# Kernel optimization log

Measured on AMD Instinct MI355X. Metric: run time of the kernel, lower is better.

## Reference

```python
import jax, jax.numpy as jnp
import numpy as np

N_HEADS = 12


def setup_inputs() -> dict:
    key = jax.random.key(0)
    ks = jax.random.split(key, 4)
    B, T, C = 1, 4096, 768
    x = jax.random.normal(ks[0], (B, T, C), dtype=jnp.float32)
    w_qkv = jax.random.normal(ks[1], (C, 3 * C), dtype=jnp.float32) * (C ** -0.5)
    b_qkv = jnp.zeros((3 * C,), dtype=jnp.float32)
    w_proj = jax.random.normal(ks[2], (C, C), dtype=jnp.float32) * (C ** -0.5)
    b_proj = jnp.zeros((C,), dtype=jnp.float32)
    return {"x": x, "w_qkv": w_qkv, "b_qkv": b_qkv, "w_proj": w_proj, "b_proj": b_proj}


def reference(x, w_qkv, b_qkv, w_proj, b_proj):
    B, T, C = x.shape
    H = N_HEADS
    hd = C // H
    qkv = x @ w_qkv + b_qkv                      # [B,T,3C]
    q, k, v = jnp.split(qkv, 3, axis=-1)
    # [B,H,T,hd]
    q = q.reshape(B, T, H, hd).transpose(0, 2, 1, 3)
    k = k.reshape(B, T, H, hd).transpose(0, 2, 1, 3)
    v = v.reshape(B, T, H, hd).transpose(0, 2, 1, 3)
    scale = 1.0 / jnp.sqrt(jnp.float32(hd))
    attn = jnp.einsum('bhqd,bhkd->bhqk', q, k) * scale  # [B,H,T,T]
    causal = jnp.tril(jnp.ones((T, T), dtype=bool))
    attn = jnp.where(causal, attn, jnp.float32(-jnp.inf))
    attn = jax.nn.softmax(attn, axis=-1)
    out = jnp.einsum('bhqk,bhkd->bhqd', attn, v)        # [B,H,T,hd]
    out = out.transpose(0, 2, 1, 3).reshape(B, T, C)
    return out @ w_proj + b_proj
```

## Files before the change

kernel.cpp:

```cpp
#include <hip/hip_runtime.h>
#include <hip/hip_bf16.h>


#define T_SEQ 4096
#define C_DIM 768
#define C3    2304
#define NH    12
#define HD    64

typedef __attribute__((ext_vector_type(8))) short bf16x8;
typedef __attribute__((ext_vector_type(4))) short bf16x4;
typedef __attribute__((ext_vector_type(4))) float f32x4;

__device__ inline unsigned short f2bf(float f) {
  union { float f; unsigned u; } v; v.f = f;
  unsigned r = v.u + 0x7fff + ((v.u >> 16) & 1);
  return (unsigned short)(r >> 16);
}
__device__ inline unsigned pack_bf16_trunc(float a, float b) {
  union { float f; unsigned u; } x, y; x.f = a; y.f = b;
  return (x.u >> 16) | (y.u & 0xffff0000u);
}

__device__ inline void gl2lds16(const void* g, void* l) {
  __builtin_amdgcn_global_load_lds(
      (const __attribute__((address_space(1))) unsigned int*)g,
      (__attribute__((address_space(3))) unsigned int*)l, 16, 0, 0);
}

#if __has_builtin(__builtin_amdgcn_exp2f)
#define EXP2F(x) __builtin_amdgcn_exp2f(x)
#else
#define EXP2F(x) exp2f(x)
#endif

#define NB_CONV  (T_SEQ * C_DIM / 2048)
#define NB_TQKV  ((C3 / 32) * (C_DIM / 32))
#define NB_TPROJ ((C_DIM / 32) * (C_DIM / 32))

__global__ __launch_bounds__(256) void prep_fused(
    const float* __restrict__ x, const float* __restrict__ w_qkv,
    const float* __restrict__ w_proj, unsigned short* __restrict__ xb,
    unsigned short* __restrict__ wqkvT, unsigned short* __restrict__ wprojT) {
  __shared__ float t[32][33];
  const int b = blockIdx.x;
  const int tid = threadIdx.x;

  if (b < NB_CONV) {
    int i = (b * 256 + tid) * 8;
    float4 v0 = *(const float4*)(x + i);
    float4 v1 = *(const float4*)(x + i + 4);
    unsigned short o[8] = {f2bf(v0.x), f2bf(v0.y), f2bf(v0.z), f2bf(v0.w),
                           f2bf(v1.x), f2bf(v1.y), f2bf(v1.z), f2bf(v1.w)};
    *(uint4*)(xb + i) = *(uint4*)o;
    return;
  }
  const float* in;
  unsigned short* outT;
  int R, Cc, bi;
  if (b < NB_CONV + NB_TQKV) {
    in = w_qkv; outT = wqkvT; R = C_DIM; Cc = C3; bi = b - NB_CONV;
  } else {
    in = w_proj; outT = wprojT; R = C_DIM; Cc = C_DIM; bi = b - NB_CONV - NB_TQKV;
  }
  const int tx = tid & 31, ty = tid >> 5;
  const int c0 = (bi % (Cc / 32)) * 32, r0 = (bi / (Cc / 32)) * 32;
#pragma unroll
  for (int i = 0; i < 4; ++i) {
    int r = ty + i * 8;
    t[r][tx] = in[(size_t)(r0 + r) * Cc + c0 + tx];
  }
  __syncthreads();
#pragma unroll
  for (int i = 0; i < 4; ++i) {
    int c = ty + i * 8;
    outT[(size_t)(c0 + c) * R + r0 + tx] = f2bf(t[tx][c]);
  }
}

__global__ __launch_bounds__(256) void gemm_qkv(
    const unsigned short* __restrict__ A, const unsigned short* __restrict__ Bt,
    const float* __restrict__ bias, unsigned short* __restrict__ Cq,
    unsigned short* __restrict__ vTp, int M, int N, int K) {
  __shared__ unsigned short As[128 * 32];
  __shared__ unsigned short Bs[128 * 32];
  const int tid = threadIdx.x;
  const int wave = tid >> 6, lane = tid & 63;
  const int lo = lane & 15, g8 = lane >> 4;
  const int wm = wave >> 1, wn = wave & 1;
  const int bm = blockIdx.y * 128, bn = blockIdx.x * 128;
  const int lrow = lane >> 2;
  const int lcol = (lane & 3) * 8;

  f32x4 acc[4][4];
#pragma unroll
  for (int mt = 0; mt < 4; ++mt)
#pragma unroll
    for (int nt = 0; nt < 4; ++nt) acc[mt][nt] = (f32x4){0.f, 0.f, 0.f, 0.f};

  const unsigned short* Abase = A + (size_t)bm * K;
  const unsigned short* Bbase = Bt + (size_t)bn * K;

  for (int k0 = 0; k0 < K; k0 += 32) {
    __syncthreads();
#pragma unroll
    for (int c = 0; c < 2; ++c) {
      const int r = wave * 32 + c * 16;
      gl2lds16(Abase + (size_t)(r + lrow) * K + k0 + lcol, As + r * 32 + lane * 8);
      gl2lds16(Bbase + (size_t)(r + lrow) * K + k0 + lcol, Bs + r * 32 + lane * 8);
    }
    __syncthreads();

    bf16x8 a[4], b[4];
#pragma unroll
    for (int mt = 0; mt < 4; ++mt)
      a[mt] = *(const bf16x8*)(As + (wm * 64 + mt * 16 + lo) * 32 + g8 * 8);
#pragma unroll
    for (int nt = 0; nt < 4; ++nt)
      b[nt] = *(const bf16x8*)(Bs + (wn * 64 + nt * 16 + lo) * 32 + g8 * 8);
#pragma unroll
    for (int mt = 0; mt < 4; ++mt)
#pragma unroll
      for (int nt = 0; nt < 4; ++nt)
        acc[mt][nt] = __builtin_amdgcn_mfma_f32_16x16x32_bf16(a[mt], b[nt], acc[mt][nt], 0, 0, 0);
  }

  if (bn < 2 * C_DIM) {
#pragma unroll
    for (int nt = 0; nt < 4; ++nt) {
      const int n = bn + wn * 64 + nt * 16 + lo;
      const float bv = bias[n];
#pragma unroll
      for (int mt = 0; mt < 4; ++mt)
#pragma unroll
        for (int r = 0; r < 4; ++r) {
          const int m = bm + wm * 64 + mt * 16 + g8 * 4 + r;
          Cq[(size_t)m * C3 + n] = f2bf(acc[mt][nt][r] + bv);
        }
    }
  } else {
#pragma unroll
    for (int nt = 0; nt < 4; ++nt) {
      const int n = bn + wn * 64 + nt * 16 + lo;
      const float bv = bias[n];
      unsigned short* row = vTp + (size_t)(n - 2 * C_DIM) * T_SEQ;
#pragma unroll
      for (int mt = 0; mt < 4; ++mt) {
        const int mbase = (bm + wm * 64 + mt * 16 + g8 * 4) & ~31;
        bf16x4 o4;
#pragma unroll
        for (int r = 0; r < 4; ++r) o4[r] = (short)f2bf(acc[mt][nt][r] + bv);
        *(bf16x4*)(row + mbase + 8 * g8 + 4 * (mt & 1)) = o4;
      }
    }
  }
}

__global__ __launch_bounds__(256) void gemm_bt_mfma(
    const unsigned short* __restrict__ A, const unsigned short* __restrict__ Bt,
    const float* __restrict__ bias, float* __restrict__ C,
    int M, int N, int K) {
  __shared__ unsigned short As[128 * 32];
  __shared__ unsigned short Bs[128 * 32];
  const int tid = threadIdx.x;
  const int wave = tid >> 6, lane = tid & 63;
  const int lo = lane & 15, g8 = lane >> 4;
  const int wm = wave >> 1, wn = wave & 1;
  const int bm = blockIdx.y * 128, bn = blockIdx.x * 128;
  const int lrow = lane >> 2;
  const int lcol = (lane & 3) * 8;

  f32x4 acc[4][4];
#pragma unroll
  for (int mt = 0; mt < 4; ++mt)
#pragma unroll
    for (int nt = 0; nt < 4; ++nt) acc[mt][nt] = (f32x4){0.f, 0.f, 0.f, 0.f};

  const unsigned short* Abase = A + (size_t)bm * K;
  const unsigned short* Bbase = Bt + (size_t)bn * K;

  for (int k0 = 0; k0 < K; k0 += 32) {
    __syncthreads();
#pragma unroll
    for (int c = 0; c < 2; ++c) {
      const int r = wave * 32 + c * 16;
      gl2lds16(Abase + (size_t)(r + lrow) * K + k0 + lcol, As + r * 32 + lane * 8);
      gl2lds16(Bbase + (size_t)(r + lrow) * K + k0 + lcol, Bs + r * 32 + lane * 8);
    }
    __syncthreads();

    bf16x8 a[4], b[4];
#pragma unroll
    for (int mt = 0; mt < 4; ++mt)
      a[mt] = *(const bf16x8*)(As + (wm * 64 + mt * 16 + lo) * 32 + g8 * 8);
#pragma unroll
    for (int nt = 0; nt < 4; ++nt)
      b[nt] = *(const bf16x8*)(Bs + (wn * 64 + nt * 16 + lo) * 32 + g8 * 8);
#pragma unroll
    for (int mt = 0; mt < 4; ++mt)
#pragma unroll
      for (int nt = 0; nt < 4; ++nt)
        acc[mt][nt] = __builtin_amdgcn_mfma_f32_16x16x32_bf16(a[mt], b[nt], acc[mt][nt], 0, 0, 0);
  }

#pragma unroll
  for (int nt = 0; nt < 4; ++nt) {
    const int n = bn + wn * 64 + nt * 16 + lo;
    const float bv = bias[n];
#pragma unroll
    for (int mt = 0; mt < 4; ++mt)
#pragma unroll
      for (int r = 0; r < 4; ++r) {
        const int m = bm + wm * 64 + mt * 16 + g8 * 4 + r;
        C[(size_t)m * N + n] = acc[mt][nt][r] + bv;
      }
  }
}

__global__ __launch_bounds__(256) void flash_attn_mfma10(
    const unsigned short* __restrict__ qkv,
    const unsigned short* __restrict__ vTp,
    unsigned short* __restrict__ out) {
  __shared__ unsigned short Ks[2][64 * 64];
  __shared__ unsigned short Vs[2][64 * 64];

  const int bx = blockIdx.x;
  const int bin = bx & 255, role = bx >> 8;
  const int s = bin >> 6, r_ = bin & 63, half = r_ >> 5, j = r_ & 31;
  int v_, h;
  if (role == 0)      { v_ = 64 - j;           h = 2 * s + half; }
  else if (role == 1) { v_ = 32 - j;           h = 2 * s + half; }
  else                { v_ = 2 * j + 1 + half; h = 8 + s; }
  const int qt = v_ - 1;
  const int q0 = qt * 64;
  const int tid = threadIdx.x;
  const int w = tid >> 6;
  const int lane = tid & 63;
  const int lo = lane & 15;
  const int g = lane >> 4;
  const int lo7 = lo & 7;
  const float qscale = 0.125f * 1.44269504f;

  const unsigned short* Kg = qkv + C_DIM + h * HD;
  const unsigned short* Vg = vTp + (size_t)(h * HD) * T_SEQ;

  const int drow = tid >> 3;
  const int dslot = (tid & 7) * 8;
  const int dsrc = ((tid & 7) ^ (drow & 7)) * 8;

  bf16x8 qb[2];
#pragma unroll
  for (int dh = 0; dh < 2; ++dh)
    qb[dh] = *(const bf16x8*)(
        qkv + (size_t)(q0 + w * 16 + lo) * C3 + h * HD + dh * 32 + g * 8);

#pragma unroll
  for (int p = 0; p < 2; ++p) {
    const int r = p * 32 + drow;
    gl2lds16(Kg + (size_t)r * C3 + dsrc, Ks[0] + r * 64 + dslot);
    gl2lds16(Vg + (size_t)r * T_SEQ + dsrc, Vs[0] + r * 64 + dslot);
  }
  __syncthreads();

  float l_i = 0.f;
  f32x4 o_acc[4];
#pragma unroll
  for (int dt = 0; dt < 4; ++dt) o_acc[dt] = (f32x4){0.f, 0.f, 0.f, 0.f};

  for (int t = 0; t <= qt; ++t) {
    const int cur = t & 1;
    if (t < qt) {
      const int k0n = (t + 1) * 64;
#pragma unroll
      for (int p = 0; p < 2; ++p) {
        const int r = p * 32 + drow;
        gl2lds16(Kg + (size_t)(k0n + r) * C3 + dsrc, Ks[cur ^ 1] + r * 64 + dslot);
        gl2lds16(Vg + (size_t)r * T_SEQ + k0n + dsrc, Vs[cur ^ 1] + r * 64 + dslot);
      }
    }

    f32x4 st[4];
#pragma unroll
    for (int mt = 0; mt < 4; ++mt) st[mt] = (f32x4){0.f, 0.f, 0.f, 0.f};
#pragma unroll
    for (int mt = 0; mt < 4; ++mt)
#pragma unroll
      for (int dh = 0; dh < 2; ++dh) {
        bf16x8 a = *(const bf16x8*)(
            Ks[cur] + (mt * 16 + lo) * 64 + (((dh * 4 + g) ^ lo7) * 8));
        st[mt] = __builtin_amdgcn_mfma_f32_16x16x32_bf16(a, qb[dh], st[mt], 0, 0, 0);
      }

    if (t == qt) {
      const int qloc = w * 16 + lo;
#pragma unroll
      for (int mt = 0; mt < 4; ++mt)
#pragma unroll
        for (int r = 0; r < 4; ++r)
          if (mt * 16 + g * 4 + r > qloc) st[mt][r] = -1e30f;
    }

    float lsum = 0.f;
    union { bf16x8 v; unsigned u[4]; } pt[2];
#pragma unroll
    for (int kh = 0; kh < 2; ++kh) {
      float e0 = EXP2F(st[kh * 2][0] * qscale);
      float e1 = EXP2F(st[kh * 2][1] * qscale);
      float e2 = EXP2F(st[kh * 2][2] * qscale);
      float e3 = EXP2F(st[kh * 2][3] * qscale);
      float f0 = EXP2F(st[kh * 2 + 1][0] * qscale);
      float f1 = EXP2F(st[kh * 2 + 1][1] * qscale);
      float f2 = EXP2F(st[kh * 2 + 1][2] * qscale);
      float f3 = EXP2F(st[kh * 2 + 1][3] * qscale);
      lsum += (e0 + e1) + (e2 + e3) + (f0 + f1) + (f2 + f3);
      pt[kh].u[0] = pack_bf16_trunc(e0, e1);
      pt[kh].u[1] = pack_bf16_trunc(e2, e3);
      pt[kh].u[2] = pack_bf16_trunc(f0, f1);
      pt[kh].u[3] = pack_bf16_trunc(f2, f3);
    }
    l_i += lsum;

#pragma unroll
    for (int dt = 0; dt < 4; ++dt)
#pragma unroll
      for (int kh = 0; kh < 2; ++kh) {
        bf16x8 av = *(const bf16x8*)(
            Vs[cur] + (dt * 16 + lo) * 64 + (((kh * 4 + g) ^ lo7) * 8));
        o_acc[dt] = __builtin_amdgcn_mfma_f32_16x16x32_bf16(av, pt[kh].v, o_acc[dt], 0, 0, 0);
      }

    __syncthreads();
  }

  l_i += __shfl_xor(l_i, 16);
  l_i += __shfl_xor(l_i, 32);
  const float inv = 1.0f / l_i;
  unsigned short* Es = Ks[0];
#pragma unroll
  for (int dt = 0; dt < 4; ++dt) {
    const int chunk = (dt * 2 + (g >> 1)) ^ lo7;
#pragma unroll
    for (int r = 0; r < 4; ++r)
      Es[(w * 16 + lo) * 64 + chunk * 8 + (g & 1) * 4 + r] =
          f2bf(o_acc[dt][r] * inv);
  }
#pragma unroll
  for (int i = 0; i < 2; ++i) {
    const int row = w * 16 + i * 8 + (lane >> 3);
    bf16x8 val = *(const bf16x8*)(Es + row * 64 + (((lane & 7) ^ (row & 7)) * 8));
    *(bf16x8*)(out + (size_t)(q0 + row) * C_DIM + h * HD + (lane & 7) * 8) = val;
  }
}

extern "C" void kernel_launch(void* const* d_in, const int* in_sizes, int n_in,
                              void* d_out, int out_size, void* d_ws, size_t ws_size,
                              hipStream_t stream) {
  const float* x      = (const float*)d_in[0];
  const float* w_qkv  = (const float*)d_in[1];
  const float* b_qkv  = (const float*)d_in[2];
  const float* w_proj = (const float*)d_in[3];
  const float* b_proj = (const float*)d_in[4];
  float* out = (float*)d_out;

  unsigned short* xb     = (unsigned short*)d_ws;
  unsigned short* wqkvT  = xb + (size_t)T_SEQ * C_DIM;
  unsigned short* wprojT = wqkvT + (size_t)C3 * C_DIM;
  unsigned short* qkv    = wprojT + (size_t)C_DIM * C_DIM;
  unsigned short* vTp    = qkv + (size_t)T_SEQ * C3;
  unsigned short* attnb  = vTp + (size_t)C_DIM * T_SEQ;

  prep_fused<<<NB_CONV + NB_TQKV + NB_TPROJ, 256, 0, stream>>>(
      x, w_qkv, w_proj, xb, wqkvT, wprojT);

  gemm_qkv<<<dim3(C3 / 128, T_SEQ / 128), 256, 0, stream>>>(
      xb, wqkvT, b_qkv, qkv, vTp, T_SEQ, C3, C_DIM);

  flash_attn_mfma10<<<T_SEQ / 64 * NH, 256, 0, stream>>>(qkv, vTp, attnb);

  gemm_bt_mfma<<<dim3(C_DIM / 128, T_SEQ / 128), 256, 0, stream>>>(
      attnb, wprojT, b_proj, out, T_SEQ, C_DIM, C_DIM);
}
```

Baseline: 209.0 us.

## Double GEMM K-tile to 64 with XOR-swizzled LDS and simplify attention block order

```diff
diff --git a/kernel.cpp b/kernel.cpp
--- a/kernel.cpp
+++ b/kernel.cpp
@@ -82,15 +82,17 @@
     const unsigned short* __restrict__ A, const unsigned short* __restrict__ Bt,
     const float* __restrict__ bias, unsigned short* __restrict__ Cq,
     unsigned short* __restrict__ vTp, int M, int N, int K) {
-  __shared__ unsigned short As[128 * 32];
-  __shared__ unsigned short Bs[128 * 32];
+  __shared__ unsigned short As[128 * 64];
+  __shared__ unsigned short Bs[128 * 64];
   const int tid = threadIdx.x;
   const int wave = tid >> 6, lane = tid & 63;
   const int lo = lane & 15, g8 = lane >> 4;
+  const int lo7 = lo & 7;
   const int wm = wave >> 1, wn = wave & 1;
   const int bm = blockIdx.y * 128, bn = blockIdx.x * 128;
-  const int lrow = lane >> 2;
-  const int lcol = (lane & 3) * 8;
+  const int drow8 = lane >> 3;
+  const int dslot = (lane & 7) * 8;
+  const int dsrc = ((lane & 7) ^ drow8) * 8;
 
   f32x4 acc[4][4];
 #pragma unroll
@@ -101,28 +103,33 @@
   const unsigned short* Abase = A + (size_t)bm * K;
   const unsigned short* Bbase = Bt + (size_t)bn * K;
 
-  for (int k0 = 0; k0 < K; k0 += 32) {
-    __syncthreads();
-#pragma unroll
-    for (int c = 0; c < 2; ++c) {
-      const int r = wave * 32 + c * 16;
-      gl2lds16(Abase + (size_t)(r + lrow) * K + k0 + lcol, As + r * 32 + lane * 8);
-      gl2lds16(Bbase + (size_t)(r + lrow) * K + k0 + lcol, Bs + r * 32 + lane * 8);
-    }
-    __syncthreads();
-
-    bf16x8 a[4], b[4];
-#pragma unroll
-    for (int mt = 0; mt < 4; ++mt)
-      a[mt] = *(const bf16x8*)(As + (wm * 64 + mt * 16 + lo) * 32 + g8 * 8);
-#pragma unroll
-    for (int nt = 0; nt < 4; ++nt)
-      b[nt] = *(const bf16x8*)(Bs + (wn * 64 + nt * 16 + lo) * 32 + g8 * 8);
-#pragma unroll
-    for (int mt = 0; mt < 4; ++mt)
+  for (int k0 = 0; k0 < K; k0 += 64) {
+    __syncthreads();
+#pragma unroll
+    for (int p = 0; p < 4; ++p) {
+      const int r = p * 32 + wave * 8 + drow8;
+      gl2lds16(Abase + (size_t)r * K + k0 + dsrc, As + r * 64 + dslot);
+      gl2lds16(Bbase + (size_t)r * K + k0 + dsrc, Bs + r * 64 + dslot);
+    }
+    __syncthreads();
+
+#pragma unroll
+    for (int kk = 0; kk < 2; ++kk) {
+      bf16x8 a[4], b[4];
+#pragma unroll
+      for (int mt = 0; mt < 4; ++mt)
+        a[mt] = *(const bf16x8*)(
+            As + (wm * 64 + mt * 16 + lo) * 64 + (((kk * 4 + g8) ^ lo7) * 8));
 #pragma unroll
       for (int nt = 0; nt < 4; ++nt)
-        acc[mt][nt] = __builtin_amdgcn_mfma_f32_16x16x32_bf16(a[mt], b[nt], acc[mt][nt], 0, 0, 0);
+        b[nt] = *(const bf16x8*)(
+            Bs + (wn * 64 + nt * 16 + lo) * 64 + (((kk * 4 + g8) ^ lo7) * 8));
+#pragma unroll
+      for (int mt = 0; mt < 4; ++mt)
+#pragma unroll
+        for (int nt = 0; nt < 4; ++nt)
+          acc[mt][nt] = __builtin_amdgcn_mfma_f32_16x16x32_bf16(a[mt], b[nt], acc[mt][nt], 0, 0, 0);
+    }
   }
 
   if (bn < 2 * C_DIM) {
@@ -160,15 +167,17 @@
     const unsigned short* __restrict__ A, const unsigned short* __restrict__ Bt,
     const float* __restrict__ bias, float* __restrict__ C,
     int M, int N, int K) {
-  __shared__ unsigned short As[128 * 32];
-  __shared__ unsigned short Bs[128 * 32];
+  __shared__ unsigned short As[128 * 64];
+  __shared__ unsigned short Bs[128 * 64];
   const int tid = threadIdx.x;
   const int wave = tid >> 6, lane = tid & 63;
   const int lo = lane & 15, g8 = lane >> 4;
+  const int lo7 = lo & 7;
   const int wm = wave >> 1, wn = wave & 1;
   const int bm = blockIdx.y * 128, bn = blockIdx.x * 128;
-  const int lrow = lane >> 2;
-  const int lcol = (lane & 3) * 8;
+  const int drow8 = lane >> 3;
+  const int dslot = (lane & 7) * 8;
+  const int dsrc = ((lane & 7) ^ drow8) * 8;
 
   f32x4 acc[4][4];
 #pragma unroll
@@ -179,28 +188,33 @@
   const unsigned short* Abase = A + (size_t)bm * K;
   const unsigned short* Bbase = Bt + (size_t)bn * K;
 
-  for (int k0 = 0; k0 < K; k0 += 32) {
-    __syncthreads();
-#pragma unroll
-    for (int c = 0; c < 2; ++c) {
-      const int r = wave * 32 + c * 16;
-      gl2lds16(Abase + (size_t)(r + lrow) * K + k0 + lcol, As + r * 32 + lane * 8);
-      gl2lds16(Bbase + (size_t)(r + lrow) * K + k0 + lcol, Bs + r * 32 + lane * 8);
-    }
-    __syncthreads();
-
-    bf16x8 a[4], b[4];
-#pragma unroll
-    for (int mt = 0; mt < 4; ++mt)
-      a[mt] = *(const bf16x8*)(As + (wm * 64 + mt * 16 + lo) * 32 + g8 * 8);
-#pragma unroll
-    for (int nt = 0; nt < 4; ++nt)
-      b[nt] = *(const bf16x8*)(Bs + (wn * 64 + nt * 16 + lo) * 32 + g8 * 8);
-#pragma unroll
-    for (int mt = 0; mt < 4; ++mt)
+  for (int k0 = 0; k0 < K; k0 += 64) {
+    __syncthreads();
+#pragma unroll
+    for (int p = 0; p < 4; ++p) {
+      const int r = p * 32 + wave * 8 + drow8;
+      gl2lds16(Abase + (size_t)r * K + k0 + dsrc, As + r * 64 + dslot);
+      gl2lds16(Bbase + (size_t)r * K + k0 + dsrc, Bs + r * 64 + dslot);
+    }
+    __syncthreads();
+
+#pragma unroll
+    for (int kk = 0; kk < 2; ++kk) {
+      bf16x8 a[4], b[4];
+#pragma unroll
+      for (int mt = 0; mt < 4; ++mt)
+        a[mt] = *(const bf16x8*)(
+            As + (wm * 64 + mt * 16 + lo) * 64 + (((kk * 4 + g8) ^ lo7) * 8));
 #pragma unroll
       for (int nt = 0; nt < 4; ++nt)
-        acc[mt][nt] = __builtin_amdgcn_mfma_f32_16x16x32_bf16(a[mt], b[nt], acc[mt][nt], 0, 0, 0);
+        b[nt] = *(const bf16x8*)(
+            Bs + (wn * 64 + nt * 16 + lo) * 64 + (((kk * 4 + g8) ^ lo7) * 8));
+#pragma unroll
+      for (int mt = 0; mt < 4; ++mt)
+#pragma unroll
+        for (int nt = 0; nt < 4; ++nt)
+          acc[mt][nt] = __builtin_amdgcn_mfma_f32_16x16x32_bf16(a[mt], b[nt], acc[mt][nt], 0, 0, 0);
+    }
   }
 
 #pragma unroll
@@ -217,21 +231,15 @@
   }
 }
 
-__global__ __launch_bounds__(256) void flash_attn_mfma10(
+__global__ __launch_bounds__(256) void flash_attn_mfma11(
     const unsigned short* __restrict__ qkv,
     const unsigned short* __restrict__ vTp,
     unsigned short* __restrict__ out) {
   __shared__ unsigned short Ks[2][64 * 64];
   __shared__ unsigned short Vs[2][64 * 64];
 
-  const int bx = blockIdx.x;
-  const int bin = bx & 255, role = bx >> 8;
-  const int s = bin >> 6, r_ = bin & 63, half = r_ >> 5, j = r_ & 31;
-  int v_, h;
-  if (role == 0)      { v_ = 64 - j;           h = 2 * s + half; }
-  else if (role == 1) { v_ = 32 - j;           h = 2 * s + half; }
-  else                { v_ = 2 * j + 1 + half; h = 8 + s; }
-  const int qt = v_ - 1;
+  const int qt = 63 - blockIdx.x / NH;
+  const int h = blockIdx.x % NH;
   const int q0 = qt * 64;
   const int tid = threadIdx.x;
   const int w = tid >> 6;
@@ -375,7 +383,7 @@
   gemm_qkv<<<dim3(C3 / 128, T_SEQ / 128), 256, 0, stream>>>(
       xb, wqkvT, b_qkv, qkv, vTp, T_SEQ, C3, C_DIM);
 
-  flash_attn_mfma10<<<T_SEQ / 64 * NH, 256, 0, stream>>>(qkv, vTp, attnb);
+  flash_attn_mfma11<<<T_SEQ / 64 * NH, 256, 0, stream>>>(qkv, vTp, attnb);
 
   gemm_bt_mfma<<<dim3(C_DIM / 128, T_SEQ / 128), 256, 0, stream>>>(
       attnb, wprojT, b_proj, out, T_SEQ, C_DIM, C_DIM);
```

After: 195.8 us. 6.3% less time.
